# Kernel tuning notes

Hardware: AMD Instinct MI355X
Metric: run time of the kernel (lower is better)

The kernel has to match this reference:

```python
import jax, jax.numpy as jnp
import numpy as np

B, S, D, H = 4, 2048, 1024, 16
HD = D // H


def setup_inputs() -> dict:
    key = jax.random.key(0)
    ks = jax.random.split(key, 12)
    inp = {
        'query': jax.random.normal(ks[0], (B, S, D), jnp.float32),
        'key': jax.random.normal(ks[1], (B, S, D), jnp.float32),
        'value': jax.random.normal(ks[2], (B, S, D), jnp.float32),
        'mask': jnp.ones((B, 1, 1, S), jnp.bool_),
        # nn.Linear weights are [out, in]; y = x @ W.T + b
        'Wq': jax.random.normal(ks[3], (D, D), jnp.float32) * 0.02,
        'bq': jnp.zeros((D,), jnp.float32),
        'Wk': jax.random.normal(ks[4], (D, D), jnp.float32) * 0.02,
        'bk': jnp.zeros((D,), jnp.float32),
        'Wv': jax.random.normal(ks[5], (D, D), jnp.float32) * 0.02,
        'bv': jnp.zeros((D,), jnp.float32),
        'Wo': jax.random.normal(ks[6], (D, D), jnp.float32) * 0.02,
        'bo': jnp.zeros((D,), jnp.float32),
    }
    return inp


def reference(query, key, value, mask, Wq, bq, Wk, bk, Wv, bv, Wo, bo):
    scale = 1.0 / np.sqrt(HD).astype(np.float32)

    def proj(x, W, b):
        # [B,S,D] -> [B,H,S,HD]
        y = x @ W.T + b
        return y.reshape(B, S, H, HD).transpose(0, 2, 1, 3)

    q = proj(query, Wq, bq)
    k = proj(key, Wk, bk)
    v = proj(value, Wv, bv)
    # scores: [B,H,S,S]
    scores = jnp.einsum('bhqd,bhkd->bhqk', q, k) * scale
    scores = jnp.where(mask, scores, -jnp.inf)
    attn = jax.nn.softmax(scores, axis=-1)  # dropout p=0 in eval
    ctx = jnp.einsum('bhqk,bhkd->bhqd', attn, v)  # [B,H,S,HD]
    ctx = ctx.transpose(0, 2, 1, 3).reshape(B, S, D)
    return ctx @ Wo.T + bo
```

## Files before the change

kernel.cpp:

```cpp
#include <hip/hip_runtime.h>
#include <hip/hip_bf16.h>

#define SCLOG (0.125f * 1.4426950408889634f)

typedef __attribute__((ext_vector_type(8))) short short8;
typedef __attribute__((ext_vector_type(4))) short s16x4;
typedef __attribute__((ext_vector_type(4))) float f32x4;

__device__ __forceinline__ short f2bf(float f) {
    __hip_bfloat16 h = __float2bfloat16(f);
    short s;
    __builtin_memcpy(&s, &h, 2);
    return s;
}

__device__ __forceinline__ void gl_lds16(const void* g, void* l) {
    __builtin_amdgcn_global_load_lds(
        (const __attribute__((address_space(1))) unsigned int*)g,
        (__attribute__((address_space(3))) unsigned int*)l,
        16, 0, 0);
}

__global__ __launch_bounds__(256) void cvt3(
    const float* __restrict__ a, const float* __restrict__ b,
    const float* __restrict__ c, short* __restrict__ oa,
    short* __restrict__ ob, short* __restrict__ oc, int n8)
{
    int i = blockIdx.x * 256 + threadIdx.x;
    if (i >= n8) return;
    const float* in = blockIdx.y == 0 ? a : (blockIdx.y == 1 ? b : c);
    short* out = blockIdx.y == 0 ? oa : (blockIdx.y == 1 ? ob : oc);
    float4 v0 = ((const float4*)in)[2 * i];
    float4 v1 = ((const float4*)in)[2 * i + 1];
    short8 s = { f2bf(v0.x), f2bf(v0.y), f2bf(v0.z), f2bf(v0.w),
                 f2bf(v1.x), f2bf(v1.y), f2bf(v1.z), f2bf(v1.w) };
    *(short8*)(out + 8 * (size_t)i) = s;
}

__global__ __launch_bounds__(256) void cvt4(
    const float* __restrict__ a, const float* __restrict__ b,
    const float* __restrict__ c, const float* __restrict__ d,
    short* __restrict__ oa, short* __restrict__ ob,
    short* __restrict__ oc, short* __restrict__ od, int n8)
{
    int i = blockIdx.x * 256 + threadIdx.x;
    if (i >= n8) return;
    const float* in = blockIdx.y == 0 ? a : (blockIdx.y == 1 ? b :
                      (blockIdx.y == 2 ? c : d));
    short* out = blockIdx.y == 0 ? oa : (blockIdx.y == 1 ? ob :
                 (blockIdx.y == 2 ? oc : od));
    float4 v0 = ((const float4*)in)[2 * i];
    float4 v1 = ((const float4*)in)[2 * i + 1];
    short8 s = { f2bf(v0.x), f2bf(v0.y), f2bf(v0.z), f2bf(v0.w),
                 f2bf(v1.x), f2bf(v1.y), f2bf(v1.z), f2bf(v1.w) };
    *(short8*)(out + 8 * (size_t)i) = s;
}

template<int NZ, bool OUT_BF16, bool VTOUT>
__global__ __launch_bounds__(256) void gemm_bt_bf16(
    const short* __restrict__ A0, const short* __restrict__ A1,
    const short* __restrict__ A2,
    const short* __restrict__ W0, const short* __restrict__ W1,
    const short* __restrict__ W2,
    const float* __restrict__ b0, const float* __restrict__ b1,
    const float* __restrict__ b2,
    short* __restrict__ C0, short* __restrict__ C1, short* __restrict__ C2,
    void* __restrict__ Cf, int M, int N, int K)
{
    __shared__ short As[128 * 64];
    __shared__ short Bs[128 * 64];
    const int tid = threadIdx.x;
    const int wave = tid >> 6, lane = tid & 63;
    const int quad = lane >> 4, l16 = lane & 15;
    const int wm = (wave >> 1) * 64, wn = (wave & 1) * 64;
    const int bm0 = blockIdx.y * 128, bn0 = blockIdx.x * 128;
    const int rowA = lane >> 3;
    const int chunkS = (((lane & 7) ^ rowA) * 8);
    const int rsw = (l16 & 7);

    const short* A; const short* W; const float* bias; short* Cb;
    if constexpr (NZ == 3) {
        A    = blockIdx.z == 0 ? A0 : (blockIdx.z == 1 ? A1 : A2);
        W    = blockIdx.z == 0 ? W0 : (blockIdx.z == 1 ? W1 : W2);
        bias = blockIdx.z == 0 ? b0 : (blockIdx.z == 1 ? b1 : b2);
        Cb   = blockIdx.z == 0 ? C0 : (blockIdx.z == 1 ? C1 : C2);
    } else {
        A = A0; W = W0; bias = b0; Cb = C0;
    }

    const short* Ab = A + (size_t)bm0 * K;
    const short* Wb = W + (size_t)bn0 * K;

    f32x4 acc[4][4] = {};

    for (int kt = 0; kt < K; kt += 64) {
        #pragma unroll
        for (int i = 0; i < 4; ++i) {
            int r0 = wave * 32 + i * 8;
            gl_lds16(Ab + (size_t)(r0 + rowA) * K + kt + chunkS, As + r0 * 64);
            gl_lds16(Wb + (size_t)(r0 + rowA) * K + kt + chunkS, Bs + r0 * 64);
        }
        __syncthreads();

        #pragma unroll
        for (int h = 0; h < 2; ++h) {
            const int slot = ((h * 4 + quad) ^ rsw) * 8;
            short8 af[4], bf[4];
            #pragma unroll
            for (int mi = 0; mi < 4; ++mi)
                af[mi] = *(const short8*)(As + (wm + mi * 16 + l16) * 64 + slot);
            #pragma unroll
            for (int ni = 0; ni < 4; ++ni)
                bf[ni] = *(const short8*)(Bs + (wn + ni * 16 + l16) * 64 + slot);
            #pragma unroll
            for (int mi = 0; mi < 4; ++mi)
                #pragma unroll
                for (int ni = 0; ni < 4; ++ni)
                    acc[mi][ni] = __builtin_amdgcn_mfma_f32_16x16x32_bf16(
                        af[mi], bf[ni], acc[mi][ni], 0, 0, 0);
        }
        __syncthreads();
    }

    bool vt_mode = false;
    if constexpr (VTOUT) vt_mode = (blockIdx.z == 2);

    if (vt_mode) {
        const int SS = 2048;
        const int bidx = bm0 >> 11;
        const int s0b  = (bm0 & 2047) + wm;
        #pragma unroll
        for (int ni = 0; ni < 4; ++ni) {
            int n = bn0 + wn + ni * 16 + l16;
            float bb = bias[n];
            int hh = n >> 6, dd = n & 63;
            short* vrow = Cb + ((size_t)((bidx * 16 + hh) * 64 + dd)) * SS;
            #pragma unroll
            for (int mi = 0; mi < 4; ++mi) {
                int s0 = s0b + mi * 16 + quad * 4;
                s16x4 pk = { f2bf(acc[mi][ni][0] + bb), f2bf(acc[mi][ni][1] + bb),
                             f2bf(acc[mi][ni][2] + bb), f2bf(acc[mi][ni][3] + bb) };
                *(s16x4*)(vrow + s0) = pk;
            }
        }
    } else {
        #pragma unroll
        for (int ni = 0; ni < 4; ++ni) {
            int n = bn0 + wn + ni * 16 + l16;
            float bb = bias[n];
            #pragma unroll
            for (int mi = 0; mi < 4; ++mi)
                #pragma unroll
                for (int r = 0; r < 4; ++r) {
                    int m = bm0 + wm + mi * 16 + quad * 4 + r;
                    float v = acc[mi][ni][r] + bb;
                    if constexpr (OUT_BF16)
                        Cb[(size_t)m * N + n] = f2bf(v);
                    else
                        ((float*)Cf)[(size_t)m * N + n] = v;
                }
        }
    }
}

__global__ __launch_bounds__(256) void flash_attn(
    const short* __restrict__ Q, const short* __restrict__ Kb,
    const short* __restrict__ VT, const int* __restrict__ mask,
    short* __restrict__ Ctx)
{
    const int S = 2048, D = 1024;
    __shared__ short Ks[64 * 64];
    __shared__ short Vs[64 * 64];
    __shared__ short Ps[4][32 * 72];

    const int tid = threadIdx.x;
    const int wave = tid >> 6, lane = tid & 63;
    const int quad = lane >> 4, l16 = lane & 15;
    const int q0 = blockIdx.x * 128 + wave * 32;
    const int head = blockIdx.y, b = blockIdx.z;
    const size_t qbase  = ((size_t)(b * S)) * D + head * 64;
    const size_t vtbase = ((size_t)((b * 16 + head) * 64)) * S;
    const int rowA = lane >> 3;
    const int chunkS = (((lane & 7) ^ rowA) * 8);
    const int rsw = (l16 & 7);

    short8 qf[2][2];
    #pragma unroll
    for (int qi = 0; qi < 2; ++qi)
        #pragma unroll
        for (int h = 0; h < 2; ++h)
            qf[qi][h] = *(const short8*)(Q + qbase + (size_t)(q0 + qi * 16 + l16) * D + h * 32 + quad * 8);

    f32x4 o[2][4] = {};
    f32x4 osum[2] = {};
    const short8 ones = { (short)0x3F80, (short)0x3F80, (short)0x3F80, (short)0x3F80,
                          (short)0x3F80, (short)0x3F80, (short)0x3F80, (short)0x3F80 };

    const int* mrow = mask + (size_t)b * S;
    short* Pw = Ps[wave];
    const int slot0 = (quad ^ rsw) * 8;
    const int slot1 = ((4 + quad) ^ rsw) * 8;

    for (int kt = 0; kt < S; kt += 64) {
        __syncthreads();
        {
            int r0 = wave * 16;
            gl_lds16(Kb + qbase + (size_t)(kt + r0 + rowA) * D + chunkS, Ks + r0 * 64);
            gl_lds16(Kb + qbase + (size_t)(kt + r0 + 8 + rowA) * D + chunkS, Ks + (r0 + 8) * 64);
            gl_lds16(VT + vtbase + (size_t)(r0 + rowA) * S + kt + chunkS, Vs + r0 * 64);
            gl_lds16(VT + vtbase + (size_t)(r0 + 8 + rowA) * S + kt + chunkS, Vs + (r0 + 8) * 64);
        }
        __syncthreads();

        float p[2][4][4];
        #pragma unroll
        for (int t = 0; t < 4; ++t) {
            short8 kf0 = *(const short8*)(Ks + (t * 16 + l16) * 64 + slot0);
            short8 kf1 = *(const short8*)(Ks + (t * 16 + l16) * 64 + slot1);
            float mb = mrow[kt + t * 16 + l16] != 0 ? 0.f : -1e30f;
            #pragma unroll
            for (int qi = 0; qi < 2; ++qi) {
                f32x4 a = {};
                a = __builtin_amdgcn_mfma_f32_16x16x32_bf16(qf[qi][0], kf0, a, 0, 0, 0);
                a = __builtin_amdgcn_mfma_f32_16x16x32_bf16(qf[qi][1], kf1, a, 0, 0, 0);
                #pragma unroll
                for (int r = 0; r < 4; ++r)
                    p[qi][t][r] = __builtin_amdgcn_exp2f(__builtin_fmaf(a[r], SCLOG, mb));
            }
        }

        #pragma unroll
        for (int qi = 0; qi < 2; ++qi)
            #pragma unroll
            for (int t = 0; t < 4; ++t)
                #pragma unroll
                for (int r = 0; r < 4; ++r)
                    Pw[(qi * 16 + quad * 4 + r) * 72 + t * 16 + l16] = f2bf(p[qi][t][r]);

        __builtin_amdgcn_s_setprio(1);
        #pragma unroll
        for (int h = 0; h < 2; ++h) {
            const int vslot = ((h * 4 + quad) ^ rsw) * 8;
            short8 pa0 = *(const short8*)(Pw + l16 * 72 + h * 32 + quad * 8);
            short8 pa1 = *(const short8*)(Pw + (16 + l16) * 72 + h * 32 + quad * 8);
            osum[0] = __builtin_amdgcn_mfma_f32_16x16x32_bf16(pa0, ones, osum[0], 0, 0, 0);
            osum[1] = __builtin_amdgcn_mfma_f32_16x16x32_bf16(pa1, ones, osum[1], 0, 0, 0);
            #pragma unroll
            for (int nt = 0; nt < 4; ++nt) {
                short8 bv = *(const short8*)(Vs + (nt * 16 + l16) * 64 + vslot);
                o[0][nt] = __builtin_amdgcn_mfma_f32_16x16x32_bf16(pa0, bv, o[0][nt], 0, 0, 0);
                o[1][nt] = __builtin_amdgcn_mfma_f32_16x16x32_bf16(pa1, bv, o[1][nt], 0, 0, 0);
            }
        }
        __builtin_amdgcn_s_setprio(0);
    }

    float inv[2][4];
    #pragma unroll
    for (int qi = 0; qi < 2; ++qi)
        #pragma unroll
        for (int r = 0; r < 4; ++r)
            inv[qi][r] = 1.0f / osum[qi][r];

    #pragma unroll
    for (int qi = 0; qi < 2; ++qi)
        #pragma unroll
        for (int nt = 0; nt < 4; ++nt)
            #pragma unroll
            for (int r = 0; r < 4; ++r) {
                float v = o[qi][nt][r] * inv[qi][r];
                Ctx[qbase + (size_t)(q0 + qi * 16 + quad * 4 + r) * D + nt * 16 + l16] = f2bf(v);
            }
}

extern "C" void kernel_launch(void* const* d_in, const int* in_sizes, int n_in,
                              void* d_out, int out_size, void* d_ws, size_t ws_size,
                              hipStream_t stream) {
    const int B = 4, S = 2048, D = 1024, H = 16;
    const int M = B * S;
    const size_t MD = (size_t)M * D;

    const float* q_in = (const float*)d_in[0];
    const float* k_in = (const float*)d_in[1];
    const float* v_in = (const float*)d_in[2];
    const int* mask = (const int*)d_in[3];
    const float* Wq = (const float*)d_in[4];
    const float* bq = (const float*)d_in[5];
    const float* Wk = (const float*)d_in[6];
    const float* bk = (const float*)d_in[7];
    const float* Wv = (const float*)d_in[8];
    const float* bv = (const float*)d_in[9];
    const float* Wo = (const float*)d_in[10];
    const float* bo = (const float*)d_in[11];

    short* S1 = (short*)d_ws;
    short* S2 = S1 + MD;
    short* S3 = S2 + MD;
    short* S4 = S3 + MD;
    short* wqb = S4 + MD;
    short* wkb = wqb + (size_t)D * D;
    short* wvb = wkb + (size_t)D * D;
    short* wob = wvb + (size_t)D * D;
    short* S5 = wob + (size_t)D * D;
    short* S6 = S5 + MD;

    short *qbf = S1, *kbf = S2, *vbf = S3;
    short *Qb = S4, *Kb2 = S5, *VTb = S6, *Ctx = S2;

    dim3 blk(256);
    int n8_in = (int)(MD / 8);
    int n8_w  = D * D / 8;
    cvt3<<<dim3((n8_in + 255) / 256, 3), blk, 0, stream>>>(
        q_in, k_in, v_in, qbf, kbf, vbf, n8_in);
    cvt4<<<dim3((n8_w + 255) / 256, 4), blk, 0, stream>>>(
        Wq, Wk, Wv, Wo, wqb, wkb, wvb, wob, n8_w);

    dim3 g1(D / 128, M / 128, 3);
    gemm_bt_bf16<3, true, true><<<g1, blk, 0, stream>>>(
        qbf, kbf, vbf, wqb, wkb, wvb, bq, bk, bv,
        Qb, Kb2, VTb, nullptr, M, D, D);

    dim3 g2(S / 128, H, B);
    flash_attn<<<g2, blk, 0, stream>>>(Qb, Kb2, VTb, mask, Ctx);

    dim3 g3(D / 128, M / 128, 1);
    gemm_bt_bf16<1, false, false><<<g3, blk, 0, stream>>>(
        Ctx, nullptr, nullptr, wob, nullptr, nullptr, bo, nullptr, nullptr,
        nullptr, nullptr, nullptr, (float*)d_out, M, D, D);
}
```

Measured before the change: 398.0 us.

## Halve per-wave query rows in flash attention and compute row sums with shuffles

Each wave now handles 16 query rows instead of 32, so the attention grid doubles to S/64 blocks along the query axis. The row-sum normaliser is accumulated in fp32 registers and reduced with xor shuffles instead of an extra MFMA against a ones vector, and the s_setprio hints are removed. This is meant to raise occupancy and cut MFMA work for the denominator. In exchange, K/V tiles are loaded into LDS twice as often per query row, which raises memory traffic.

```diff
diff --git a/kernel.cpp b/kernel.cpp
--- a/kernel.cpp
+++ b/kernel.cpp
@@ -171,12 +171,12 @@
     const int S = 2048, D = 1024;
     __shared__ short Ks[64 * 64];
     __shared__ short Vs[64 * 64];
-    __shared__ short Ps[4][32 * 72];
+    __shared__ short Ps[4][16 * 72];
 
     const int tid = threadIdx.x;
     const int wave = tid >> 6, lane = tid & 63;
     const int quad = lane >> 4, l16 = lane & 15;
-    const int q0 = blockIdx.x * 128 + wave * 32;
+    const int q0 = blockIdx.x * 64 + wave * 16;
     const int head = blockIdx.y, b = blockIdx.z;
     const size_t qbase  = ((size_t)(b * S)) * D + head * 64;
     const size_t vtbase = ((size_t)((b * 16 + head) * 64)) * S;
@@ -184,17 +184,13 @@
     const int chunkS = (((lane & 7) ^ rowA) * 8);
     const int rsw = (l16 & 7);
 
-    short8 qf[2][2];
+    short8 qf[2];
     #pragma unroll
-    for (int qi = 0; qi < 2; ++qi)
-        #pragma unroll
-        for (int h = 0; h < 2; ++h)
-            qf[qi][h] = *(const short8*)(Q + qbase + (size_t)(q0 + qi * 16 + l16) * D + h * 32 + quad * 8);
-
-    f32x4 o[2][4] = {};
-    f32x4 osum[2] = {};
-    const short8 ones = { (short)0x3F80, (short)0x3F80, (short)0x3F80, (short)0x3F80,
-                          (short)0x3F80, (short)0x3F80, (short)0x3F80, (short)0x3F80 };
+    for (int h = 0; h < 2; ++h)
+        qf[h] = *(const short8*)(Q + qbase + (size_t)(q0 + l16) * D + h * 32 + quad * 8);
+
+    f32x4 o[4] = {};
+    float ls[4] = {};
 
     const int* mrow = mask + (size_t)b * S;
     short* Pw = Ps[wave];
@@ -212,65 +208,57 @@
         }
         __syncthreads();
 
-        float p[2][4][4];
+        float p[4][4];
         #pragma unroll
         for (int t = 0; t < 4; ++t) {
             short8 kf0 = *(const short8*)(Ks + (t * 16 + l16) * 64 + slot0);
             short8 kf1 = *(const short8*)(Ks + (t * 16 + l16) * 64 + slot1);
             float mb = mrow[kt + t * 16 + l16] != 0 ? 0.f : -1e30f;
-            #pragma unroll
-            for (int qi = 0; qi < 2; ++qi) {
-                f32x4 a = {};
-                a = __builtin_amdgcn_mfma_f32_16x16x32_bf16(qf[qi][0], kf0, a, 0, 0, 0);
-                a = __builtin_amdgcn_mfma_f32_16x16x32_bf16(qf[qi][1], kf1, a, 0, 0, 0);
-                #pragma unroll
-                for (int r = 0; r < 4; ++r)
-                    p[qi][t][r] = __builtin_amdgcn_exp2f(__builtin_fmaf(a[r], SCLOG, mb));
+            f32x4 a = {};
+            a = __builtin_amdgcn_mfma_f32_16x16x32_bf16(qf[0], kf0, a, 0, 0, 0);
+            a = __builtin_amdgcn_mfma_f32_16x16x32_bf16(qf[1], kf1, a, 0, 0, 0);
+            #pragma unroll
+            for (int r = 0; r < 4; ++r) {
+                float pv = __builtin_amdgcn_exp2f(__builtin_fmaf(a[r], SCLOG, mb));
+                p[t][r] = pv;
+                ls[r] += pv;
             }
         }
 
         #pragma unroll
-        for (int qi = 0; qi < 2; ++qi)
-            #pragma unroll
-            for (int t = 0; t < 4; ++t)
-                #pragma unroll
-                for (int r = 0; r < 4; ++r)
-                    Pw[(qi * 16 + quad * 4 + r) * 72 + t * 16 + l16] = f2bf(p[qi][t][r]);
-
-        __builtin_amdgcn_s_setprio(1);
+        for (int t = 0; t < 4; ++t)
+            #pragma unroll
+            for (int r = 0; r < 4; ++r)
+                Pw[(quad * 4 + r) * 72 + t * 16 + l16] = f2bf(p[t][r]);
+
         #pragma unroll
         for (int h = 0; h < 2; ++h) {
             const int vslot = ((h * 4 + quad) ^ rsw) * 8;
-            short8 pa0 = *(const short8*)(Pw + l16 * 72 + h * 32 + quad * 8);
-            short8 pa1 = *(const short8*)(Pw + (16 + l16) * 72 + h * 32 + quad * 8);
-            osum[0] = __builtin_amdgcn_mfma_f32_16x16x32_bf16(pa0, ones, osum[0], 0, 0, 0);
-            osum[1] = __builtin_amdgcn_mfma_f32_16x16x32_bf16(pa1, ones, osum[1], 0, 0, 0);
+            short8 pa = *(const short8*)(Pw + l16 * 72 + h * 32 + quad * 8);
             #pragma unroll
             for (int nt = 0; nt < 4; ++nt) {
                 short8 bv = *(const short8*)(Vs + (nt * 16 + l16) * 64 + vslot);
-                o[0][nt] = __builtin_amdgcn_mfma_f32_16x16x32_bf16(pa0, bv, o[0][nt], 0, 0, 0);
-                o[1][nt] = __builtin_amdgcn_mfma_f32_16x16x32_bf16(pa1, bv, o[1][nt], 0, 0, 0);
+                o[nt] = __builtin_amdgcn_mfma_f32_16x16x32_bf16(pa, bv, o[nt], 0, 0, 0);
             }
         }
-        __builtin_amdgcn_s_setprio(0);
-    }
-
-    float inv[2][4];
+    }
+
     #pragma unroll
-    for (int qi = 0; qi < 2; ++qi)
-        #pragma unroll
-        for (int r = 0; r < 4; ++r)
-            inv[qi][r] = 1.0f / osum[qi][r];
+    for (int r = 0; r < 4; ++r) {
+        float v = ls[r];
+        #pragma unroll
+        for (int off = 1; off < 16; off <<= 1)
+            v += __shfl_xor(v, off, 64);
+        ls[r] = 1.0f / v;
+    }
 
     #pragma unroll
-    for (int qi = 0; qi < 2; ++qi)
-        #pragma unroll
-        for (int nt = 0; nt < 4; ++nt)
-            #pragma unroll
-            for (int r = 0; r < 4; ++r) {
-                float v = o[qi][nt][r] * inv[qi][r];
-                Ctx[qbase + (size_t)(q0 + qi * 16 + quad * 4 + r) * D + nt * 16 + l16] = f2bf(v);
-            }
+    for (int nt = 0; nt < 4; ++nt)
+        #pragma unroll
+        for (int r = 0; r < 4; ++r) {
+            float v = o[nt][r] * ls[r];
+            Ctx[qbase + (size_t)(q0 + quad * 4 + r) * D + nt * 16 + l16] = f2bf(v);
+        }
 }
 
 extern "C" void kernel_launch(void* const* d_in, const int* in_sizes, int n_in,
@@ -320,7 +308,7 @@
         qbf, kbf, vbf, wqb, wkb, wvb, bq, bk, bv,
         Qb, Kb2, VTb, nullptr, M, D, D);
 
-    dim3 g2(S / 128, H, B);
+    dim3 g2(S / 64, H, B);
     flash_attn<<<g2, blk, 0, stream>>>(Qb, Kb2, VTb, mask, Ctx);
 
     dim3 g3(D / 128, M / 128, 1);
```

New measurement: 400.5 us. About the same (+0.6%).
